# Performance work log

Hardware: AMD Instinct MI355X
Metric: run time of the kernel (lower is better)

## Reference

```python
import jax, jax.numpy as jnp
import numpy as np

EPS = 1e-5  # BatchNorm1d default eps


def setup_inputs() -> dict:
    key = jax.random.key(0)
    k1, k2, k3 = jax.random.split(key, 3)
    N, C, H, W = 8, 64, 256, 256
    K = 16  # instances per image
    x = jax.random.normal(k1, (N, C, H, W), dtype=jnp.float32)
    ins_indices_batch = jax.random.randint(k2, (N, H, W), 0, K, dtype=jnp.int64)
    gamma = jnp.ones((C,), dtype=jnp.float32) + 0.1 * jax.random.normal(k3, (C,), dtype=jnp.float32)
    beta = jnp.zeros((C,), dtype=jnp.float32)
    return {"x": x, "ins_indices_batch": ins_indices_batch, "gamma": gamma, "beta": beta, "num_instances": K}


def reference(x, ins_indices_batch, gamma, beta, num_instances):
    # Fused equivalent of the per-instance gather -> BatchNorm1d(train) -> scatter loop.
    N, C, H, W = x.shape
    HW = H * W
    K = num_instances
    ids = ins_indices_batch.reshape(N, HW)                     # [N, HW]
    xv = x.reshape(N, C, HW).transpose(0, 2, 1).reshape(N * HW, C)  # pixels x channels
    valid = (ids >= 0).reshape(-1)                              # -1 ids are skipped (unchanged)
    seg = (jnp.arange(N, dtype=ids.dtype)[:, None] * K + jnp.clip(ids, 0, K - 1)).reshape(-1)
    seg = seg.astype(jnp.int32)
    w = valid.astype(xv.dtype)[:, None]                         # [N*HW, 1]
    nseg = N * K
    cnt = jax.ops.segment_sum(w, seg, num_segments=nseg)        # [nseg, 1]
    s = jax.ops.segment_sum(xv * w, seg, num_segments=nseg)     # [nseg, C]
    ss = jax.ops.segment_sum(xv * xv * w, seg, num_segments=nseg)
    denom = jnp.maximum(cnt, 1.0)
    mean = s / denom                                            # per-(image,instance,channel)
    var = ss / denom - mean * mean                              # biased var (BN training stats)
    xn = (xv - mean[seg]) * jax.lax.rsqrt(var[seg] + EPS) * gamma + beta
    out = jnp.where(valid[:, None], xn, xv)
    return out.reshape(N, HW, C).transpose(0, 2, 1).reshape(N, C, H, W)
```

## Files before the change

kernel.cpp:

```cpp
#include <hip/hip_runtime.h>
#include <hip/hip_bf16.h>
#include <stdint.h>

#define N_IMG 8
#define K_INS 16
#define CCH   64
#define SB    256
#define PXC   256
#define EPSV  1e-5f

typedef float vfloat4 __attribute__((ext_vector_type(4)));
typedef short bf16x8 __attribute__((ext_vector_type(8)));
typedef float f32x4 __attribute__((ext_vector_type(4)));

#define P_OFF    0
#define P2_OFF   16777216
#define SCSH_OFF 16908288

__device__ __forceinline__ short bf16_bits(float v) {
    __hip_bfloat16 h = __float2bfloat16(v);
    union { __hip_bfloat16 h; short s; } u;
    u.h = h;
    return u.s;
}

__global__ __launch_bounds__(256) void stats_kernel(const float* __restrict__ x,
                                                    const int* __restrict__ ids,
                                                    float2* __restrict__ P,
                                                    float* __restrict__ P2, int HW) {
    const int n = blockIdx.x;
    const int sb = blockIdx.y;
    const int t = threadIdx.x;
    const int wave = t >> 6;
    const int lane = t & 63;
    const int row = lane & 15;
    const int kg = lane >> 4;

    const int chunk = HW / SB;
    const float* xrow = x + (size_t)(n * CCH + wave * 16 + row) * HW + sb * chunk;
    const int* idp = ids + (size_t)n * HW + sb * chunk;

    f32x4 accS = {0.f, 0.f, 0.f, 0.f};
    f32x4 accQ = {0.f, 0.f, 0.f, 0.f};
    f32x4 accC = {0.f, 0.f, 0.f, 0.f};
    bf16x8 ones;
#pragma unroll
    for (int j = 0; j < 8; ++j) ones[j] = (short)0x3F80;

#pragma unroll
    for (int s = 0; s < chunk / 32; ++s) {
        const int p = s * 32 + kg * 8;
        float4 xa = *(const float4*)(xrow + p);
        float4 xb = *(const float4*)(xrow + p + 4);
        int4 ia = *(const int4*)(idp + p);
        int4 ib = *(const int4*)(idp + p + 4);
        float xs[8] = {xa.x, xa.y, xa.z, xa.w, xb.x, xb.y, xb.z, xb.w};
        int iv[8] = {ia.x, ia.y, ia.z, ia.w, ib.x, ib.y, ib.z, ib.w};
        bf16x8 ax, aq, mk;
#pragma unroll
        for (int j = 0; j < 8; ++j) {
            ax[j] = bf16_bits(xs[j]);
            aq[j] = bf16_bits(xs[j] * xs[j]);
            mk[j] = (iv[j] == row) ? (short)0x3F80 : (short)0;
        }
        accS = __builtin_amdgcn_mfma_f32_16x16x32_bf16(ax, mk, accS, 0, 0, 0);
        accQ = __builtin_amdgcn_mfma_f32_16x16x32_bf16(aq, mk, accQ, 0, 0, 0);
        accC = __builtin_amdgcn_mfma_f32_16x16x32_bf16(ones, mk, accC, 0, 0, 0);
    }

    float2* Pb = P + (size_t)((n * 4 + wave) * SB + sb) * 256;
#pragma unroll
    for (int r = 0; r < 4; ++r) {
        Pb[(kg * 4 + r) * 16 + row] = make_float2(accS[r], accQ[r]);
    }
    if (t < 16) P2[((size_t)n * SB + sb) * 16 + t] = accC[0];
}

__global__ __launch_bounds__(256) void finalize_kernel(const float2* __restrict__ P,
                                                       const float* __restrict__ P2,
                                                       const float* __restrict__ gamma,
                                                       const float* __restrict__ beta,
                                                       float2* __restrict__ scsh) {
    const int cb = blockIdx.x;
    const int n = blockIdx.y;
    const int t = threadIdx.x;

    __shared__ float csh[16][17];
    const float* P2n = P2 + (size_t)n * SB * 16;
    float cc = 0.f;
#pragma unroll 4
    for (int i = 0; i < 16; ++i) cc += P2n[((t >> 4) * 16 + i) * 16 + (t & 15)];
    csh[t >> 4][t & 15] = cc;

    const float2* Pb = P + (size_t)(n * 4 + cb) * SB * 256;
    float rs = 0.f, rq = 0.f;
#pragma unroll 16
    for (int sb = 0; sb < SB; ++sb) {
        float2 v = Pb[(size_t)sb * 256 + t];
        rs += v.x;
        rq += v.y;
    }
    __syncthreads();
    float cnt = 0.f;
#pragma unroll
    for (int i = 0; i < 16; ++i) cnt += csh[i][t & 15];

    const int c = cb * 16 + (t >> 4);
    const int k = t & 15;
    float denom = fmaxf(cnt, 1.0f);
    float mean = rs / denom;
    float var = rq / denom - mean * mean;
    float r = rsqrtf(var + EPSV);
    float sc = r * gamma[c];
    float sh = beta[c] - mean * sc;
    scsh[((size_t)n * CCH + c) * K_INS + k] = make_float2(sc, sh);
}

__global__ __launch_bounds__(256) void norm_kernel(const float* __restrict__ x,
                                                   const int* __restrict__ ids,
                                                   const float2* __restrict__ scsh,
                                                   float* __restrict__ out, int HW) {
    const int sb = blockIdx.x;
    const int n = blockIdx.y;
    const int t = threadIdx.x;
    const int lane = t & 63;
    const int wave = t >> 6;
    const int px0 = sb * PXC;

    int4 myid = *(const int4*)(ids + (size_t)n * HW + px0 + lane * 4);

    __shared__ float2 ls[CCH * K_INS];
    const float4* src = (const float4*)(scsh + (size_t)n * CCH * K_INS);
    ((float4*)ls)[t] = src[t];
    ((float4*)ls)[t + 256] = src[t + 256];
    __syncthreads();

    const int i0 = max(myid.x, 0), i1 = max(myid.y, 0);
    const int i2 = max(myid.z, 0), i3 = max(myid.w, 0);

#pragma unroll 4
    for (int ci = 0; ci < 16; ++ci) {
        const int c = wave * 16 + ci;
        const float* xr = x + ((size_t)n * CCH + c) * HW + px0;
        float4 xv = *(const float4*)(xr + lane * 4);
        const float2* lc = ls + c * K_INS;
        float2 s0 = lc[i0], s1 = lc[i1], s2 = lc[i2], s3 = lc[i3];
        vfloat4 o;
        o.x = (myid.x >= 0) ? fmaf(xv.x, s0.x, s0.y) : xv.x;
        o.y = (myid.y >= 0) ? fmaf(xv.y, s1.x, s1.y) : xv.y;
        o.z = (myid.z >= 0) ? fmaf(xv.z, s2.x, s2.y) : xv.z;
        o.w = (myid.w >= 0) ? fmaf(xv.w, s3.x, s3.y) : xv.w;
        __builtin_nontemporal_store(o, (vfloat4*)(out + ((size_t)n * CCH + c) * HW + px0) + lane);
    }
}

extern "C" void kernel_launch(void* const* d_in, const int* in_sizes, int n_in,
                              void* d_out, int out_size, void* d_ws, size_t ws_size,
                              hipStream_t stream) {
    const float* x = (const float*)d_in[0];
    const int* ids = (const int*)d_in[1];
    const float* gamma = (const float*)d_in[2];
    const float* beta = (const float*)d_in[3];
    float* out = (float*)d_out;

    const int HW = in_sizes[1] / N_IMG;

    float2* P = (float2*)((char*)d_ws + P_OFF);
    float* P2 = (float*)((char*)d_ws + P2_OFF);
    float2* scsh = (float2*)((char*)d_ws + SCSH_OFF);

    stats_kernel<<<dim3(N_IMG, SB), 256, 0, stream>>>(x, ids, P, P2, HW);
    finalize_kernel<<<dim3(4, N_IMG), 256, 0, stream>>>(P, P2, gamma, beta, scsh);
    norm_kernel<<<dim3(HW / PXC, N_IMG), 256, 0, stream>>>(x, ids, scsh, out, HW);
}
```

Measured before the change: 88.71 us.

## Widen norm kernel to eight pixels per lane and hardcode stats loop count

The norm kernel now covers 512 pixels per block, with each lane loading and writing eight pixels per channel, so the grid holds half as many blocks and each block loads its per-image scale/shift table into LDS half as often. The channel loop is fully unrolled. The stats kernel loop count is fixed at 8, which matches HW/SB for 256x256 images but breaks for other sizes. Output stores change from nontemporal to ordinary stores, which may affect cache behaviour.

```diff
diff --git a/kernel.cpp b/kernel.cpp
--- a/kernel.cpp
+++ b/kernel.cpp
@@ -6,7 +6,7 @@
 #define K_INS 16
 #define CCH   64
 #define SB    256
-#define PXC   256
+#define PXC   512
 #define EPSV  1e-5f
 
 typedef float vfloat4 __attribute__((ext_vector_type(4)));
@@ -40,15 +40,16 @@
     const float* xrow = x + (size_t)(n * CCH + wave * 16 + row) * HW + sb * chunk;
     const int* idp = ids + (size_t)n * HW + sb * chunk;
 
-    f32x4 accS = {0.f, 0.f, 0.f, 0.f};
-    f32x4 accQ = {0.f, 0.f, 0.f, 0.f};
-    f32x4 accC = {0.f, 0.f, 0.f, 0.f};
     bf16x8 ones;
 #pragma unroll
     for (int j = 0; j < 8; ++j) ones[j] = (short)0x3F80;
 
+    f32x4 accS = {0.f, 0.f, 0.f, 0.f};
+    f32x4 accQ = {0.f, 0.f, 0.f, 0.f};
+    f32x4 accC = {0.f, 0.f, 0.f, 0.f};
+
 #pragma unroll
-    for (int s = 0; s < chunk / 32; ++s) {
+    for (int s = 0; s < 8; ++s) {
         const int p = s * 32 + kg * 8;
         float4 xa = *(const float4*)(xrow + p);
         float4 xb = *(const float4*)(xrow + p + 4);
@@ -127,7 +128,9 @@
     const int wave = t >> 6;
     const int px0 = sb * PXC;
 
-    int4 myid = *(const int4*)(ids + (size_t)n * HW + px0 + lane * 4);
+    const int* idbase = ids + (size_t)n * HW + px0 + lane * 8;
+    int4 ida = *(const int4*)(idbase);
+    int4 idb = *(const int4*)(idbase + 4);
 
     __shared__ float2 ls[CCH * K_INS];
     const float4* src = (const float4*)(scsh + (size_t)n * CCH * K_INS);
@@ -135,22 +138,30 @@
     ((float4*)ls)[t + 256] = src[t + 256];
     __syncthreads();
 
-    const int i0 = max(myid.x, 0), i1 = max(myid.y, 0);
-    const int i2 = max(myid.z, 0), i3 = max(myid.w, 0);
+    const int a0 = max(ida.x, 0), a1 = max(ida.y, 0), a2 = max(ida.z, 0), a3 = max(ida.w, 0);
+    const int b0 = max(idb.x, 0), b1 = max(idb.y, 0), b2 = max(idb.z, 0), b3 = max(idb.w, 0);
 
-#pragma unroll 4
+#pragma unroll
     for (int ci = 0; ci < 16; ++ci) {
         const int c = wave * 16 + ci;
-        const float* xr = x + ((size_t)n * CCH + c) * HW + px0;
-        float4 xv = *(const float4*)(xr + lane * 4);
+        const float* xr = x + ((size_t)n * CCH + c) * HW + px0 + lane * 8;
+        float4 xa = *(const float4*)(xr);
+        float4 xb = *(const float4*)(xr + 4);
         const float2* lc = ls + c * K_INS;
-        float2 s0 = lc[i0], s1 = lc[i1], s2 = lc[i2], s3 = lc[i3];
-        vfloat4 o;
-        o.x = (myid.x >= 0) ? fmaf(xv.x, s0.x, s0.y) : xv.x;
-        o.y = (myid.y >= 0) ? fmaf(xv.y, s1.x, s1.y) : xv.y;
-        o.z = (myid.z >= 0) ? fmaf(xv.z, s2.x, s2.y) : xv.z;
-        o.w = (myid.w >= 0) ? fmaf(xv.w, s3.x, s3.y) : xv.w;
-        __builtin_nontemporal_store(o, (vfloat4*)(out + ((size_t)n * CCH + c) * HW + px0) + lane);
+        float2 sa0 = lc[a0], sa1 = lc[a1], sa2 = lc[a2], sa3 = lc[a3];
+        float2 sb0 = lc[b0], sb1 = lc[b1], sb2 = lc[b2], sb3 = lc[b3];
+        vfloat4 oa, ob;
+        oa.x = (ida.x >= 0) ? fmaf(xa.x, sa0.x, sa0.y) : xa.x;
+        oa.y = (ida.y >= 0) ? fmaf(xa.y, sa1.x, sa1.y) : xa.y;
+        oa.z = (ida.z >= 0) ? fmaf(xa.z, sa2.x, sa2.y) : xa.z;
+        oa.w = (ida.w >= 0) ? fmaf(xa.w, sa3.x, sa3.y) : xa.w;
+        ob.x = (idb.x >= 0) ? fmaf(xb.x, sb0.x, sb0.y) : xb.x;
+        ob.y = (idb.y >= 0) ? fmaf(xb.y, sb1.x, sb1.y) : xb.y;
+        ob.z = (idb.z >= 0) ? fmaf(xb.z, sb2.x, sb2.y) : xb.z;
+        ob.w = (idb.w >= 0) ? fmaf(xb.w, sb3.x, sb3.y) : xb.w;
+        float* orow = out + ((size_t)n * CCH + c) * HW + px0 + lane * 8;
+        *(vfloat4*)(orow) = oa;
+        *(vfloat4*)(orow + 4) = ob;
     }
 }
 
```

Result: slower. 91.82 us (+3.5%).
